# Performance work log

Hardware: AMD Instinct MI355X
Metric: run time of the kernel (lower is better)

The kernel has to match this reference:

```python
import jax, jax.numpy as jnp
import numpy as np

T = 1.0  # temperature

def _free_energy(v, W, b, c):
    # v: [B, V]; W: [V, H]; b: [V]; c: [H]
    vW = v @ W                                  # [B, H]
    W_colsum = W.sum(axis=0)                    # [H]
    negF_normal = (v * b).sum(-1) - jax.nn.softplus(vW + c).sum(-1)
    negF_flip = ((1.0 - v) * b).sum(-1) - jax.nn.softplus(W_colsum - vW + c).sum(-1)
    negF = jnp.stack([negF_normal, negF_flip], axis=-1)  # [B, 2]
    return -T * jax.nn.logsumexp(negF / T, axis=-1)      # [B]

def _gibbs_chain(v0, W, b, c, key, k):
    B = v0.shape[0]
    key, k0 = jax.random.split(key)
    u0 = jax.random.bernoulli(k0, 0.5, (B, 1)).astype(v0.dtype)
    b_sum = b.sum()

    def step(carry, _):
        v, u, key = carry
        key, k1, k2, k3 = jax.random.split(key, 4)
        v_branch = u * v + (1.0 - u) * (1.0 - v)
        h = jax.random.bernoulli(k1, jax.nn.sigmoid(v_branch @ W + c)).astype(v.dtype)  # [B,H]
        a = h @ W.T                                                                     # [B,V]
        vb = (v * b).sum(-1)
        va = (v * a).sum(-1)
        dE = -b_sum - a.sum(-1) + 2.0 * vb + 2.0 * va
        u_new = jax.random.bernoulli(k2, jax.nn.sigmoid(dE)).astype(v.dtype)[:, None]
        v_new = jax.random.bernoulli(k3, jax.nn.sigmoid(a + b)).astype(v.dtype)
        v = u_new * v_new + (1.0 - u_new) * (1.0 - v_new)
        return (v, u_new, key), None

    (v_model, _, _), _ = jax.lax.scan(step, (v0, u0, key), None, length=k)
    return v_model

def setup_inputs() -> dict:
    key = jax.random.key(0)
    kv, kw = jax.random.split(key)
    B, V, H = 8192, 1024, 1024
    v_data = jnp.round(jax.random.uniform(kv, (B, V), dtype=jnp.float32))  # binary 0/1
    W = 0.01 * jax.random.normal(kw, (V, H), dtype=jnp.float32)
    b = jnp.zeros((V,), dtype=jnp.float32)
    c = jnp.zeros((H,), dtype=jnp.float32)
    return {"v_data": v_data, "W": W, "b": b, "c": c, "seed": 0}

def reference(v_data, W, b, c, seed):
    K = 10  # Gibbs steps
    key = jax.random.key(seed)
    v_model = _gibbs_chain(v_data, W, b, c, key, K)
    v_model = jax.lax.stop_gradient(v_model)  # .detach() in torch
    loss = _free_energy(v_data, W, b, c).mean() - _free_energy(v_model, W, b, c).mean()
    return loss
```

## Files before the change

### kernel.cpp

```cpp
#include <hip/hip_runtime.h>
#include <hip/hip_bf16.h>
#include <stdint.h>
#include <math.h>


static constexpr int Bn = 8192;
static constexpr int Vn = 1024;
static constexpr int Hn = 1024;
static constexpr int KSTEPS = 10;

typedef _Float16 f16;
typedef f16   f16x4 __attribute__((ext_vector_type(4)));
typedef f16   f16x8 __attribute__((ext_vector_type(8)));
typedef float f32x4 __attribute__((ext_vector_type(4)));

#define GLOBAL_LOAD_LDS16(g, l)                                              \
  __builtin_amdgcn_global_load_lds(                                          \
      (const __attribute__((address_space(1))) uint32_t*)(g),                \
      (__attribute__((address_space(3))) uint32_t*)(l), 16, 0, 0)

__device__ __forceinline__ uint32_t rotl32(uint32_t x, int d) {
  return (x << d) | (x >> (32 - d));
}

__device__ __forceinline__ void tf2x32(uint32_t k0, uint32_t k1,
                                       uint32_t x0, uint32_t x1,
                                       uint32_t& o0, uint32_t& o1) {
  uint32_t k2 = k0 ^ k1 ^ 0x1BD11BDAu;
#define TFR(r) { x0 += x1; x1 = rotl32(x1, (r)); x1 ^= x0; }
  x0 += k0; x1 += k1;
  TFR(13) TFR(15) TFR(26) TFR(6)
  x0 += k1; x1 += k2 + 1u;
  TFR(17) TFR(29) TFR(16) TFR(24)
  x0 += k2; x1 += k0 + 2u;
  TFR(13) TFR(15) TFR(26) TFR(6)
  x0 += k0; x1 += k1 + 3u;
  TFR(17) TFR(29) TFR(16) TFR(24)
  x0 += k1; x1 += k2 + 4u;
  TFR(13) TFR(15) TFR(26) TFR(6)
  x0 += k2; x1 += k0 + 5u;
#undef TFR
  o0 = x0; o1 = x1;
}

__device__ __forceinline__ float rng_u01(uint2 key, uint32_t idx) {
  uint32_t o0, o1;
  tf2x32(key.x, key.y, 0u, idx, o0, o1);
  uint32_t bits = o0 ^ o1;
  return __uint_as_float((bits >> 9) | 0x3F800000u) - 1.0f;
}

__device__ __forceinline__ float bern_fast(float z, float r01) {
  float e = __expf(-z);
  return (__builtin_fmaf(r01, e, r01) < 1.0f) ? 1.f : 0.f;
}
__device__ __forceinline__ float softplus_fast(float x) {
  return fmaxf(x, 0.f) + __logf(1.f + __expf(-fabsf(x)));
}

__global__ void prep_keys(const int* __restrict__ seedp, uint2* __restrict__ keys) {
  if (threadIdx.x != 0 || blockIdx.x != 0) return;
  uint32_t seed = (uint32_t)(*seedp);
  uint2 key = make_uint2(0u, seed);
  uint2 nk, kk;
  tf2x32(key.x, key.y, 0u, 0u, nk.x, nk.y);
  tf2x32(key.x, key.y, 0u, 1u, kk.x, kk.y);
  keys[0] = kk;
  key = nk;
  for (int s = 0; s < KSTEPS; ++s) {
    uint2 t0, t1, t2, t3;
    tf2x32(key.x, key.y, 0u, 0u, t0.x, t0.y);
    tf2x32(key.x, key.y, 0u, 1u, t1.x, t1.y);
    tf2x32(key.x, key.y, 0u, 2u, t2.x, t2.y);
    tf2x32(key.x, key.y, 0u, 3u, t3.x, t3.y);
    key = t0;
    keys[1 + 3*s] = t1;
    keys[2 + 3*s] = t2;
    keys[3 + 3*s] = t3;
  }
}

__global__ __launch_bounds__(256) void colsum_part(
    const float* __restrict__ W, float* __restrict__ part) {
  const int bx = blockIdx.x, t = threadIdx.x;
  float s0 = 0.f, s1 = 0.f, s2 = 0.f, s3 = 0.f;
#pragma unroll
  for (int r = 0; r < 16; ++r) {
    const float* row = W + (size_t)(bx * 16 + r) * Hn;
    s0 += row[t]; s1 += row[t + 256]; s2 += row[t + 512]; s3 += row[t + 768];
  }
  float* p = part + (size_t)bx * Hn;
  p[t] = s0; p[t + 256] = s1; p[t + 512] = s2; p[t + 768] = s3;
}

__global__ __launch_bounds__(256) void colsum_red(
    const float* __restrict__ part, float* __restrict__ cs) {
  const int col = blockIdx.x * 256 + threadIdx.x;
  float s = 0.f;
#pragma unroll
  for (int k = 0; k < 64; ++k) s += part[(size_t)k * Hn + col];
  cs[col] = s;
}

__global__ void bsum_k(const float* __restrict__ bvec, float* __restrict__ bs) {
  __shared__ float sb[4];
  float s = 0.f;
  for (int i = threadIdx.x; i < Vn; i += 256) s += bvec[i];
  for (int off = 32; off > 0; off >>= 1) s += __shfl_down(s, off, 64);
  int wv = threadIdx.x >> 6, ln = threadIdx.x & 63;
  if (ln == 0) sb[wv] = s;
  __syncthreads();
  if (threadIdx.x == 0) bs[0] = sb[0] + sb[1] + sb[2] + sb[3];
}

__global__ __launch_bounds__(256) void cast_W(
    const float* __restrict__ W, f16* __restrict__ Wf, f16* __restrict__ WTf) {
  __shared__ f16 tile[64][65];
  const int j0 = blockIdx.x * 64, i0 = blockIdx.y * 64;
  const int tx = threadIdx.x & 63, tg = threadIdx.x >> 6;
#pragma unroll 4
  for (int rr = 0; rr < 16; ++rr) {
    const int row = tg * 16 + rr;
    float w = W[(size_t)(i0 + row) * Hn + j0 + tx];
    f16 hw = (f16)w;
    Wf[(size_t)(i0 + row) * Hn + j0 + tx] = hw;
    tile[row][tx] = hw;
  }
  __syncthreads();
#pragma unroll 4
  for (int rr = 0; rr < 16; ++rr) {
    const int row = tg * 16 + rr;
    WTf[(size_t)(j0 + row) * Vn + i0 + tx] = tile[tx][row];
  }
}

__global__ void u0_init(const uint2* __restrict__ keys, float* __restrict__ u) {
  int b = blockIdx.x * 256 + threadIdx.x;
  float r01 = rng_u01(keys[0], (uint32_t)b);
  u[b] = (r01 < 0.5f) ? 1.f : 0.f;
}

__global__ __launch_bounds__(256) void cast_vx(
    const float* __restrict__ vd, const float* __restrict__ u,
    f16* __restrict__ x) {
  const int idx = blockIdx.x * 256 + threadIdx.x;
  const int row = idx >> 8;
  const float uo = u[row];
  const float4 d = ((const float4*)vd)[idx];
  f16x4 o;
  if (uo > 0.5f) { o[0]=(f16)d.x; o[1]=(f16)d.y; o[2]=(f16)d.z; o[3]=(f16)d.w; }
  else { o[0]=(f16)(1.f-d.x); o[1]=(f16)(1.f-d.y); o[2]=(f16)(1.f-d.z); o[3]=(f16)(1.f-d.w); }
  *(f16x4*)(x + (size_t)idx * 4) = o;
}

template <int EPI>
__global__ __launch_bounds__(256, 8) void gemm_s(
    const f16* __restrict__ A, const f16* __restrict__ Bm,
    f16* __restrict__ outA, f16* __restrict__ outH,
    const f16* __restrict__ xold, f16* __restrict__ xnew,
    const float* __restrict__ bvec, const float* __restrict__ cvec,
    float* __restrict__ pA, float* __restrict__ pXA, float* __restrict__ pXB,
    const uint2* __restrict__ keys, int keyIdx)
{
  constexpr int N = 1024, K = 1024, BK = 64;
  __shared__ alignas(16) f16 As[64 * BK];
  __shared__ alignas(16) f16 Bs[64 * BK];

  const int t = threadIdx.x, wave = t >> 6, lane = t & 63;
  const int l15 = lane & 15, quad = lane >> 4;
  const int m0 = blockIdx.x * 64, n0 = blockIdx.y * 64;
  const int wm = (wave >> 1) * 32, wn = (wave & 1) * 32;

  const int rbase = lane >> 3;
  const int gch   = (lane & 7) ^ rbase;
  const f16* gA = A  + (size_t)(m0 + wave * 16 + rbase) * K + gch * 8;
  const f16* gB = Bm + (size_t)(n0 + wave * 16 + rbase) * K + gch * 8;
  f16* lA = As + wave * 16 * BK;
  f16* lB = Bs + wave * 16 * BK;

  const int swz = l15 & 7;
  const int oA  = (wm + l15) * BK;
  const int oB  = (wn + l15) * BK;

  f32x4 acc[2][2] = {};

  for (int k0 = 0; k0 < K; k0 += BK) {
    GLOBAL_LOAD_LDS16(gA + k0,         lA);
    GLOBAL_LOAD_LDS16(gA + k0 + 8 * K, lA + 8 * BK);
    GLOBAL_LOAD_LDS16(gB + k0,         lB);
    GLOBAL_LOAD_LDS16(gB + k0 + 8 * K, lB + 8 * BK);
    __syncthreads();

#pragma unroll
    for (int kc = 0; kc < 2; ++kc) {
      const int fc = ((kc * 4 + quad) ^ swz) * 8;
      f16x8 af[2], bf[2];
#pragma unroll
      for (int i = 0; i < 2; ++i) {
        af[i] = *(const f16x8*)(&As[oA + i * 16 * BK + fc]);
        bf[i] = *(const f16x8*)(&Bs[oB + i * 16 * BK + fc]);
      }
#pragma unroll
      for (int mt = 0; mt < 2; ++mt)
#pragma unroll
        for (int nt = 0; nt < 2; ++nt)
          acc[mt][nt] = __builtin_amdgcn_mfma_f32_16x16x32_f16(af[mt], bf[nt], acc[mt][nt], 0, 0, 0);
    }
    __syncthreads();
  }

  if constexpr (EPI == 0 || EPI == 1 || EPI == 2) {
    const uint2 key = (EPI != 0) ? keys[keyIdx] : make_uint2(0u, 0u);
#pragma unroll
    for (int mt = 0; mt < 2; ++mt)
#pragma unroll
      for (int r = 0; r < 4; ++r) {
        const int gm = m0 + wm + mt * 16 + quad * 4 + r;
#pragma unroll
        for (int nt = 0; nt < 2; ++nt) {
          const int gn = n0 + wn + nt * 16 + l15;
          const float val = acc[mt][nt][r];
          if constexpr (EPI == 0 || EPI == 2)
            outA[(size_t)gm * N + gn] = (f16)val;
          if constexpr (EPI == 1 || EPI == 2) {
            float z   = val + cvec[gn];
            float r01 = rng_u01(key, (uint32_t)(gm * N + gn));
            outH[(size_t)gm * N + gn] = (f16)bern_fast(z, r01);
          }
        }
      }
  } else {
    const uint2 key = keys[keyIdx];
    float bb[2];
#pragma unroll
    for (int nt = 0; nt < 2; ++nt) bb[nt] = bvec[n0 + wn + nt * 16 + l15];
#pragma unroll
    for (int mt = 0; mt < 2; ++mt)
#pragma unroll
      for (int r = 0; r < 4; ++r) {
        const int gm = m0 + wm + mt * 16 + quad * 4 + r;
        float pa = 0.f, pxa = 0.f, pxb = 0.f;
#pragma unroll
        for (int nt = 0; nt < 2; ++nt) {
          const int gn = n0 + wn + nt * 16 + l15;
          const float aval = acc[mt][nt][r];
          const float xo   = (float)xold[(size_t)gm * N + gn];
          pa  += aval;
          pxa += xo * aval;
          pxb += xo * bb[nt];
          float r01 = rng_u01(key, (uint32_t)(gm * N + gn));
          xnew[(size_t)gm * N + gn] = (f16)bern_fast(aval + bb[nt], r01);
        }
#pragma unroll
        for (int m = 1; m < 16; m <<= 1) {
          pa  += __shfl_xor(pa,  m, 64);
          pxa += __shfl_xor(pxa, m, 64);
          pxb += __shfl_xor(pxb, m, 64);
        }
        if (l15 == 0) {
          const int slot = blockIdx.y * 2 + (wave & 1);
          pA [(size_t)gm * 32 + slot] = pa;
          pXA[(size_t)gm * 32 + slot] = pxa;
          pXB[(size_t)gm * 32 + slot] = pxb;
        }
      }
  }
}

__global__ __launch_bounds__(256) void u_chain(
    const float* __restrict__ pA, const float* __restrict__ pXA,
    const float* __restrict__ pXB, const float* __restrict__ bsum,
    const uint2* __restrict__ keys, float* __restrict__ u)
{
  const int t = threadIdx.x, wave = t >> 6, lane = t & 63;
  const int r2 = lane >> 5, slot = lane & 31;
  const int row = blockIdx.x * 8 + wave * 2 + r2;
  const float bs = bsum[0];
  float uo = u[row];
  for (int s = 0; s < KSTEPS; ++s) {
    const size_t o = (size_t)s * 32 * Bn + (size_t)row * 32 + slot;
    float sa  = pA [o];
    float sxa = pXA[o];
    float sxb = pXB[o];
#pragma unroll
    for (int m = 1; m < 32; m <<= 1) {
      sa  += __shfl_xor(sa,  m, 64);
      sxa += __shfl_xor(sxa, m, 64);
      sxb += __shfl_xor(sxb, m, 64);
    }
    const float va = (uo > 0.5f) ? sxa : sa - sxa;
    const float vb = (uo > 0.5f) ? sxb : bs - sxb;
    const float dE = -bs - sa + 2.f * vb + 2.f * va;
    uo = bern_fast(dE, rng_u01(keys[2 + 3 * s], (uint32_t)row));
  }
  if (slot == 0) u[row] = uo;
}

__global__ __launch_bounds__(256) void fe_rows(
    const f16* __restrict__ araw, const f16* __restrict__ x,
    const float* __restrict__ u,
    const float* __restrict__ bvec, const float* __restrict__ cvec,
    const float* __restrict__ colsum, const float* __restrict__ bsum,
    float* __restrict__ Fout)
{
  __shared__ float s1[4], s2[4], s3[4];
  const int row = blockIdx.x;
  const int t = threadIdx.x;
  const float uo = u[row];
  const f16x4  a4 = *(const f16x4*)(araw + (size_t)row * Hn + t * 4);
  const float4 c4 = ((const float4*)cvec)[t];
  const float4 w4 = ((const float4*)colsum)[t];
  const float4 b4 = ((const float4*)bvec)[t];
  const f16x4  x4 = *(const f16x4*)(x + (size_t)row * Vn + t * 4);

  float aa[4] = { (float)a4[0], (float)a4[1], (float)a4[2], (float)a4[3] };
  float cc[4] = { c4.x, c4.y, c4.z, c4.w };
  float ww[4] = { w4.x, w4.y, w4.z, w4.w };
  float bb[4] = { b4.x, b4.y, b4.z, b4.w };
  float S1 = 0.f, S2 = 0.f, xb = 0.f;
#pragma unroll
  for (int j = 0; j < 4; ++j) {
    float m = (uo > 0.5f) ? aa[j] : ww[j] - aa[j];
    S1 += softplus_fast(m + cc[j]);
    S2 += softplus_fast(ww[j] - m + cc[j]);
    xb += (float)x4[j] * bb[j];
  }
#pragma unroll
  for (int off = 32; off > 0; off >>= 1) {
    S1 += __shfl_down(S1, off, 64);
    S2 += __shfl_down(S2, off, 64);
    xb += __shfl_down(xb, off, 64);
  }
  const int wv = t >> 6, ln = t & 63;
  if (ln == 0) { s1[wv] = S1; s2[wv] = S2; s3[wv] = xb; }
  __syncthreads();
  if (t == 0) {
    S1 = s1[0] + s1[1] + s1[2] + s1[3];
    S2 = s2[0] + s2[1] + s2[2] + s2[3];
    xb = s3[0] + s3[1] + s3[2] + s3[3];
    float vb = (uo > 0.5f) ? xb : bsum[0] - xb;
    float negn = vb - S1;
    float negf = (bsum[0] - vb) - S2;
    float mx = fmaxf(negn, negf);
    Fout[row] = -(mx + logf(expf(negn - mx) + expf(negf - mx)));
  }
}

__global__ __launch_bounds__(256) void finalize_k(
    const float* __restrict__ Fd, const float* __restrict__ Fm, float* __restrict__ out)
{
  __shared__ double sb[8];
  double sd = 0.0, sm = 0.0;
  for (int i = threadIdx.x; i < Bn; i += 256) { sd += (double)Fd[i]; sm += (double)Fm[i]; }
  for (int off = 32; off > 0; off >>= 1) { sd += __shfl_down(sd, off, 64); sm += __shfl_down(sm, off, 64); }
  const int wv = threadIdx.x >> 6, ln = threadIdx.x & 63;
  if (ln == 0) { sb[wv] = sd; sb[4 + wv] = sm; }
  __syncthreads();
  if (threadIdx.x == 0) {
    sd = sb[0] + sb[1] + sb[2] + sb[3];
    sm = sb[4] + sb[5] + sb[6] + sb[7];
    out[0] = (float)((sd - sm) / (double)Bn);
  }
}

extern "C" void kernel_launch(void* const* d_in, const int* in_sizes, int n_in,
                              void* d_out, int out_size, void* d_ws, size_t ws_size,
                              hipStream_t stream) {
  const float* v_data = (const float*)d_in[0];
  const float* W      = (const float*)d_in[1];
  const float* bvec   = (const float*)d_in[2];
  const float* cvec   = (const float*)d_in[3];
  const int*   seedp  = (const int*)d_in[4];
  float* out = (float*)d_out;

  char* ws = (char*)d_ws;
  size_t off = 0;
  auto alloc = [&](size_t bytes) -> void* {
    void* p = ws + off;
    off += (bytes + 255) & ~(size_t)255;
    return p;
  };
  f16*   xb0  = (f16*)alloc((size_t)Bn * Vn * 2);
  f16*   xb1  = (f16*)alloc((size_t)Bn * Vn * 2);
  f16*   h    = (f16*)alloc((size_t)Bn * Hn * 2);
  f16*   araw = (f16*)alloc((size_t)Bn * Hn * 2);
  f16*   Wf   = (f16*)alloc((size_t)Vn * Hn * 2);
  f16*   WTf  = (f16*)alloc((size_t)Vn * Hn * 2);
  float* cpart  = (float*)alloc(64 * Hn * 4);
  float* colsum = (float*)alloc(Hn * 4);
  float* bsum   = (float*)alloc(256);
  uint2* keys   = (uint2*)alloc(64 * sizeof(uint2));
  float* u      = (float*)alloc(Bn * 4);
  float* pA     = (float*)alloc((size_t)KSTEPS * 32 * Bn * 4);
  float* pXA    = (float*)alloc((size_t)KSTEPS * 32 * Bn * 4);
  float* pXB    = (float*)alloc((size_t)KSTEPS * 32 * Bn * 4);
  float* Fd     = (float*)alloc(Bn * 4);
  float* Fm     = (float*)alloc(Bn * 4);
  (void)ws_size; (void)in_sizes; (void)n_in; (void)out_size;

  prep_keys<<<1, 64, 0, stream>>>(seedp, keys);
  colsum_part<<<64, 256, 0, stream>>>(W, cpart);
  colsum_red<<<4, 256, 0, stream>>>(cpart, colsum);
  bsum_k<<<1, 256, 0, stream>>>(bvec, bsum);
  cast_W<<<dim3(Hn / 64, Vn / 64), 256, 0, stream>>>(W, Wf, WTf);
  u0_init<<<Bn / 256, 256, 0, stream>>>(keys, u);
  cast_vx<<<(Bn * Vn / 4) / 256, 256, 0, stream>>>(v_data, u, xb0);

  dim3 gg(Bn / 64, Hn / 64);
  f16* xs[2] = { xb0, xb1 };

  gemm_s<2><<<gg, 256, 0, stream>>>(xb0, WTf, araw, h, nullptr, nullptr,
                                    nullptr, cvec, nullptr, nullptr, nullptr, keys, 1);
  fe_rows<<<Bn, 256, 0, stream>>>(araw, xb0, u, bvec, cvec, colsum, bsum, Fd);

  for (int s = 0; s < KSTEPS; ++s) {
    if (s > 0) {
      gemm_s<1><<<gg, 256, 0, stream>>>(xs[s & 1], WTf, nullptr, h, nullptr,
                                        nullptr, nullptr, cvec, nullptr, nullptr,
                                        nullptr, keys, 1 + 3 * s);
    }
    const size_t so = (size_t)s * 32 * Bn;
    gemm_s<3><<<gg, 256, 0, stream>>>(h, Wf, nullptr, nullptr, xs[s & 1],
                                      xs[(s + 1) & 1], bvec, nullptr,
                                      pA + so, pXA + so, pXB + so, keys, 3 + 3 * s);
  }

  gemm_s<0><<<gg, 256, 0, stream>>>(xs[KSTEPS & 1], WTf, araw, nullptr, nullptr,
                                    nullptr, nullptr, nullptr, nullptr, nullptr,
                                    nullptr, keys, 0);
  u_chain<<<Bn / 8, 256, 0, stream>>>(pA, pXA, pXB, bsum, keys, u);
  fe_rows<<<Bn, 256, 0, stream>>>(araw, xs[KSTEPS & 1], u, bvec, cvec, colsum, bsum, Fm);

  finalize_k<<<1, 256, 0, stream>>>(Fd, Fm, out);
}
```

Measured before the change: 947.2 us.

## Fuse free-energy softplus sums and u-chain partials into GEMM epilogues

The free-energy softplus reductions move into the epilogues of the first and final v@W GEMMs, which removes the raw activation buffer write and the separate fe_rows passes. The u-chain partial sums are reformulated as h·colsum and h·(vW), computed in the h-sampling epilogue, so the W^T GEMM epilogue no longer reads the old x. The x·b partials are computed where x is produced, including in the cast kernel. This removes several full B×H fp16 reads and writes, at the cost of heavier epilogues with more transcendentals and extra partial-sum buffers.

Result: no change. 941.0 us (-0.7%).

```diff
diff --git a/kernel.cpp b/kernel.cpp
--- a/kernel.cpp
+++ b/kernel.cpp
@@ -134,32 +134,39 @@
   }
 }
 
-__global__ void u0_init(const uint2* __restrict__ keys, float* __restrict__ u) {
+__global__ void u0_init(const uint2* __restrict__ keys, float* __restrict__ u0) {
   int b = blockIdx.x * 256 + threadIdx.x;
   float r01 = rng_u01(keys[0], (uint32_t)b);
-  u[b] = (r01 < 0.5f) ? 1.f : 0.f;
+  u0[b] = (r01 < 0.5f) ? 1.f : 0.f;
 }
 
 __global__ __launch_bounds__(256) void cast_vx(
-    const float* __restrict__ vd, const float* __restrict__ u,
-    f16* __restrict__ x) {
-  const int idx = blockIdx.x * 256 + threadIdx.x;
-  const int row = idx >> 8;
-  const float uo = u[row];
-  const float4 d = ((const float4*)vd)[idx];
-  f16x4 o;
-  if (uo > 0.5f) { o[0]=(f16)d.x; o[1]=(f16)d.y; o[2]=(f16)d.z; o[3]=(f16)d.w; }
-  else { o[0]=(f16)(1.f-d.x); o[1]=(f16)(1.f-d.y); o[2]=(f16)(1.f-d.z); o[3]=(f16)(1.f-d.w); }
-  *(f16x4*)(x + (size_t)idx * 4) = o;
+    const float* __restrict__ vd, const float* __restrict__ u0,
+    const float* __restrict__ bvec, f16* __restrict__ x,
+    float* __restrict__ pXB0) {
+  const int row = blockIdx.x;
+  const int t = threadIdx.x;
+  const float uo = u0[row];
+  const float4 d  = ((const float4*)(vd + (size_t)row * Vn))[t];
+  const float4 bv = ((const float4*)bvec)[t];
+  float xv[4] = { d.x, d.y, d.z, d.w };
+  if (uo <= 0.5f) { xv[0]=1.f-xv[0]; xv[1]=1.f-xv[1]; xv[2]=1.f-xv[2]; xv[3]=1.f-xv[3]; }
+  f16x4 o = { (f16)xv[0], (f16)xv[1], (f16)xv[2], (f16)xv[3] };
+  *(f16x4*)(x + (size_t)row * Vn + t * 4) = o;
+  float xb = xv[0]*bv.x + xv[1]*bv.y + xv[2]*bv.z + xv[3]*bv.w;
+#pragma unroll
+  for (int m = 1; m < 8; m <<= 1) xb += __shfl_xor(xb, m, 64);
+  if ((t & 7) == 0) pXB0[(size_t)row * 32 + (t >> 3)] = xb;
 }
 
 template <int EPI>
 __global__ __launch_bounds__(256, 8) void gemm_s(
     const f16* __restrict__ A, const f16* __restrict__ Bm,
-    f16* __restrict__ outA, f16* __restrict__ outH,
-    const f16* __restrict__ xold, f16* __restrict__ xnew,
+    f16* __restrict__ outH, f16* __restrict__ xnew,
     const float* __restrict__ bvec, const float* __restrict__ cvec,
-    float* __restrict__ pA, float* __restrict__ pXA, float* __restrict__ pXB,
+    const float* __restrict__ colsum,
+    float* __restrict__ pA, float* __restrict__ pXA, float* __restrict__ pXBn,
+    float* __restrict__ pSA, float* __restrict__ pSB,
     const uint2* __restrict__ keys, int keyIdx)
 {
   constexpr int N = 1024, K = 1024, BK = 64;
@@ -209,27 +216,56 @@
     __syncthreads();
   }
 
-  if constexpr (EPI == 0 || EPI == 1 || EPI == 2) {
-    const uint2 key = (EPI != 0) ? keys[keyIdx] : make_uint2(0u, 0u);
+  const int slot = blockIdx.y * 2 + (wave & 1);
+
+  if constexpr (EPI == 1 || EPI == 2) {
+    const uint2 key = keys[keyIdx];
+    float csv[2], cvv[2];
+#pragma unroll
+    for (int nt = 0; nt < 2; ++nt) {
+      const int gn = n0 + wn + nt * 16 + l15;
+      csv[nt] = colsum[gn];
+      cvv[nt] = cvec[gn];
+    }
 #pragma unroll
     for (int mt = 0; mt < 2; ++mt)
 #pragma unroll
       for (int r = 0; r < 4; ++r) {
         const int gm = m0 + wm + mt * 16 + quad * 4 + r;
+        float pa = 0.f, pxa = 0.f, sa = 0.f, sb = 0.f;
 #pragma unroll
         for (int nt = 0; nt < 2; ++nt) {
           const int gn = n0 + wn + nt * 16 + l15;
           const float val = acc[mt][nt][r];
-          if constexpr (EPI == 0 || EPI == 2)
-            outA[(size_t)gm * N + gn] = (f16)val;
-          if constexpr (EPI == 1 || EPI == 2) {
-            float z   = val + cvec[gn];
-            float r01 = rng_u01(key, (uint32_t)(gm * N + gn));
-            outH[(size_t)gm * N + gn] = (f16)bern_fast(z, r01);
+          float r01 = rng_u01(key, (uint32_t)(gm * N + gn));
+          float hq  = bern_fast(val + cvv[nt], r01);
+          outH[(size_t)gm * N + gn] = (f16)hq;
+          pa  += hq * csv[nt];
+          pxa += hq * val;
+          if constexpr (EPI == 2) {
+            sa += softplus_fast(val + cvv[nt]);
+            sb += softplus_fast(csv[nt] - val + cvv[nt]);
           }
         }
+#pragma unroll
+        for (int m = 1; m < 16; m <<= 1) {
+          pa  += __shfl_xor(pa,  m, 64);
+          pxa += __shfl_xor(pxa, m, 64);
+          if constexpr (EPI == 2) {
+            sa += __shfl_xor(sa, m, 64);
+            sb += __shfl_xor(sb, m, 64);
+          }
+        }
+        if (l15 == 0) {
+          pA [(size_t)gm * 32 + slot] = pa;
+          pXA[(size_t)gm * 32 + slot] = pxa;
+          if constexpr (EPI == 2) {
+            pSA[(size_t)gm * 32 + slot] = sa;
+            pSB[(size_t)gm * 32 + slot] = sb;
+          }
+        }
       }
-  } else {
+  } else if constexpr (EPI == 3) {
     const uint2 key = keys[keyIdx];
     float bb[2];
 #pragma unroll
@@ -239,29 +275,48 @@
 #pragma unroll
       for (int r = 0; r < 4; ++r) {
         const int gm = m0 + wm + mt * 16 + quad * 4 + r;
-        float pa = 0.f, pxa = 0.f, pxb = 0.f;
+        float pxb = 0.f;
 #pragma unroll
         for (int nt = 0; nt < 2; ++nt) {
           const int gn = n0 + wn + nt * 16 + l15;
           const float aval = acc[mt][nt][r];
-          const float xo   = (float)xold[(size_t)gm * N + gn];
-          pa  += aval;
-          pxa += xo * aval;
-          pxb += xo * bb[nt];
           float r01 = rng_u01(key, (uint32_t)(gm * N + gn));
-          xnew[(size_t)gm * N + gn] = (f16)bern_fast(aval + bb[nt], r01);
+          float xq  = bern_fast(aval + bb[nt], r01);
+          xnew[(size_t)gm * N + gn] = (f16)xq;
+          pxb += xq * bb[nt];
+        }
+#pragma unroll
+        for (int m = 1; m < 16; m <<= 1) pxb += __shfl_xor(pxb, m, 64);
+        if (l15 == 0) pXBn[(size_t)gm * 32 + slot] = pxb;
+      }
+  } else {
+    float csv[2], cvv[2];
+#pragma unroll
+    for (int nt = 0; nt < 2; ++nt) {
+      const int gn = n0 + wn + nt * 16 + l15;
+      csv[nt] = colsum[gn];
+      cvv[nt] = cvec[gn];
+    }
+#pragma unroll
+    for (int mt = 0; mt < 2; ++mt)
+#pragma unroll
+      for (int r = 0; r < 4; ++r) {
+        const int gm = m0 + wm + mt * 16 + quad * 4 + r;
+        float sa = 0.f, sb = 0.f;
+#pragma unroll
+        for (int nt = 0; nt < 2; ++nt) {
+          const float val = acc[mt][nt][r];
+          sa += softplus_fast(val + cvv[nt]);
+          sb += softplus_fast(csv[nt] - val + cvv[nt]);
         }
 #pragma unroll
         for (int m = 1; m < 16; m <<= 1) {
-          pa  += __shfl_xor(pa,  m, 64);
-          pxa += __shfl_xor(pxa, m, 64);
-          pxb += __shfl_xor(pxb, m, 64);
+          sa += __shfl_xor(sa, m, 64);
+          sb += __shfl_xor(sb, m, 64);
         }
         if (l15 == 0) {
-          const int slot = blockIdx.y * 2 + (wave & 1);
-          pA [(size_t)gm * 32 + slot] = pa;
-          pXA[(size_t)gm * 32 + slot] = pxa;
-          pXB[(size_t)gm * 32 + slot] = pxb;
+          pSA[(size_t)gm * 32 + slot] = sa;
+          pSB[(size_t)gm * 32 + slot] = sb;
         }
       }
   }
@@ -270,13 +325,14 @@
 __global__ __launch_bounds__(256) void u_chain(
     const float* __restrict__ pA, const float* __restrict__ pXA,
     const float* __restrict__ pXB, const float* __restrict__ bsum,
-    const uint2* __restrict__ keys, float* __restrict__ u)
+    const uint2* __restrict__ keys, const float* __restrict__ u0,
+    float* __restrict__ uF)
 {
   const int t = threadIdx.x, wave = t >> 6, lane = t & 63;
   const int r2 = lane >> 5, slot = lane & 31;
   const int row = blockIdx.x * 8 + wave * 2 + r2;
   const float bs = bsum[0];
-  float uo = u[row];
+  float uo = u0[row];
   for (int s = 0; s < KSTEPS; ++s) {
     const size_t o = (size_t)s * 32 * Bn + (size_t)row * 32 + slot;
     float sa  = pA [o];
@@ -293,56 +349,45 @@
     const float dE = -bs - sa + 2.f * vb + 2.f * va;
     uo = bern_fast(dE, rng_u01(keys[2 + 3 * s], (uint32_t)row));
   }
-  if (slot == 0) u[row] = uo;
-}
-
-__global__ __launch_bounds__(256) void fe_rows(
-    const f16* __restrict__ araw, const f16* __restrict__ x,
-    const float* __restrict__ u,
-    const float* __restrict__ bvec, const float* __restrict__ cvec,
-    const float* __restrict__ colsum, const float* __restrict__ bsum,
-    float* __restrict__ Fout)
+  if (slot == 0) uF[row] = uo;
+}
+
+__device__ __forceinline__ float fe_eval(float SA, float SB, float xb,
+                                         float uo, float bs) {
+  float S1 = (uo > 0.5f) ? SA : SB;
+  float S2 = (uo > 0.5f) ? SB : SA;
+  float vb = (uo > 0.5f) ? xb : bs - xb;
+  float negn = vb - S1;
+  float negf = (bs - vb) - S2;
+  float mx = fmaxf(negn, negf);
+  return -(mx + logf(expf(negn - mx) + expf(negf - mx)));
+}
+
+__global__ __launch_bounds__(256) void fe_finish(
+    const float* __restrict__ SA0, const float* __restrict__ SB0,
+    const float* __restrict__ xb0,
+    const float* __restrict__ SAF, const float* __restrict__ SBF,
+    const float* __restrict__ xbF,
+    const float* __restrict__ u0, const float* __restrict__ uF,
+    const float* __restrict__ bsum,
+    float* __restrict__ Fd, float* __restrict__ Fm)
 {
-  __shared__ float s1[4], s2[4], s3[4];
-  const int row = blockIdx.x;
-  const int t = threadIdx.x;
-  const float uo = u[row];
-  const f16x4  a4 = *(const f16x4*)(araw + (size_t)row * Hn + t * 4);
-  const float4 c4 = ((const float4*)cvec)[t];
-  const float4 w4 = ((const float4*)colsum)[t];
-  const float4 b4 = ((const float4*)bvec)[t];
-  const f16x4  x4 = *(const f16x4*)(x + (size_t)row * Vn + t * 4);
-
-  float aa[4] = { (float)a4[0], (float)a4[1], (float)a4[2], (float)a4[3] };
-  float cc[4] = { c4.x, c4.y, c4.z, c4.w };
-  float ww[4] = { w4.x, w4.y, w4.z, w4.w };
-  float bb[4] = { b4.x, b4.y, b4.z, b4.w };
-  float S1 = 0.f, S2 = 0.f, xb = 0.f;
-#pragma unroll
-  for (int j = 0; j < 4; ++j) {
-    float m = (uo > 0.5f) ? aa[j] : ww[j] - aa[j];
-    S1 += softplus_fast(m + cc[j]);
-    S2 += softplus_fast(ww[j] - m + cc[j]);
-    xb += (float)x4[j] * bb[j];
-  }
-#pragma unroll
-  for (int off = 32; off > 0; off >>= 1) {
-    S1 += __shfl_down(S1, off, 64);
-    S2 += __shfl_down(S2, off, 64);
-    xb += __shfl_down(xb, off, 64);
-  }
-  const int wv = t >> 6, ln = t & 63;
-  if (ln == 0) { s1[wv] = S1; s2[wv] = S2; s3[wv] = xb; }
-  __syncthreads();
-  if (t == 0) {
-    S1 = s1[0] + s1[1] + s1[2] + s1[3];
-    S2 = s2[0] + s2[1] + s2[2] + s2[3];
-    xb = s3[0] + s3[1] + s3[2] + s3[3];
-    float vb = (uo > 0.5f) ? xb : bsum[0] - xb;
-    float negn = vb - S1;
-    float negf = (bsum[0] - vb) - S2;
-    float mx = fmaxf(negn, negf);
-    Fout[row] = -(mx + logf(expf(negn - mx) + expf(negf - mx)));
+  const int t = threadIdx.x, wave = t >> 6, lane = t & 63;
+  const int r2 = lane >> 5, slot = lane & 31;
+  const int row = blockIdx.x * 8 + wave * 2 + r2;
+  const size_t o = (size_t)row * 32 + slot;
+  const float bs = bsum[0];
+  float a0 = SA0[o], b0 = SB0[o], x0 = xb0[o];
+  float aF = SAF[o], bF = SBF[o], xF = xbF[o];
+#pragma unroll
+  for (int m = 1; m < 32; m <<= 1) {
+    a0 += __shfl_xor(a0, m, 64);  b0 += __shfl_xor(b0, m, 64);
+    x0 += __shfl_xor(x0, m, 64);  aF += __shfl_xor(aF, m, 64);
+    bF += __shfl_xor(bF, m, 64);  xF += __shfl_xor(xF, m, 64);
+  }
+  if (slot == 0) {
+    Fd[row] = fe_eval(a0, b0, x0, u0[row], bs);
+    Fm[row] = fe_eval(aF, bF, xF, uF[row], bs);
   }
 }
 
@@ -383,17 +428,21 @@
   f16*   xb0  = (f16*)alloc((size_t)Bn * Vn * 2);
   f16*   xb1  = (f16*)alloc((size_t)Bn * Vn * 2);
   f16*   h    = (f16*)alloc((size_t)Bn * Hn * 2);
-  f16*   araw = (f16*)alloc((size_t)Bn * Hn * 2);
   f16*   Wf   = (f16*)alloc((size_t)Vn * Hn * 2);
   f16*   WTf  = (f16*)alloc((size_t)Vn * Hn * 2);
   float* cpart  = (float*)alloc(64 * Hn * 4);
   float* colsum = (float*)alloc(Hn * 4);
   float* bsum   = (float*)alloc(256);
   uint2* keys   = (uint2*)alloc(64 * sizeof(uint2));
-  float* u      = (float*)alloc(Bn * 4);
+  float* u0     = (float*)alloc(Bn * 4);
+  float* uF     = (float*)alloc(Bn * 4);
   float* pA     = (float*)alloc((size_t)KSTEPS * 32 * Bn * 4);
   float* pXA    = (float*)alloc((size_t)KSTEPS * 32 * Bn * 4);
-  float* pXB    = (float*)alloc((size_t)KSTEPS * 32 * Bn * 4);
+  float* pXB    = (float*)alloc((size_t)(KSTEPS + 1) * 32 * Bn * 4);
+  float* SA0    = (float*)alloc((size_t)32 * Bn * 4);
+  float* SB0    = (float*)alloc((size_t)32 * Bn * 4);
+  float* SAF    = (float*)alloc((size_t)32 * Bn * 4);
+  float* SBF    = (float*)alloc((size_t)32 * Bn * 4);
   float* Fd     = (float*)alloc(Bn * 4);
   float* Fm     = (float*)alloc(Bn * 4);
   (void)ws_size; (void)in_sizes; (void)n_in; (void)out_size;
@@ -403,33 +452,37 @@
   colsum_red<<<4, 256, 0, stream>>>(cpart, colsum);
   bsum_k<<<1, 256, 0, stream>>>(bvec, bsum);
   cast_W<<<dim3(Hn / 64, Vn / 64), 256, 0, stream>>>(W, Wf, WTf);
-  u0_init<<<Bn / 256, 256, 0, stream>>>(keys, u);
-  cast_vx<<<(Bn * Vn / 4) / 256, 256, 0, stream>>>(v_data, u, xb0);
+  u0_init<<<Bn / 256, 256, 0, stream>>>(keys, u0);
+  cast_vx<<<Bn, 256, 0, stream>>>(v_data, u0, bvec, xb0, pXB);
 
   dim3 gg(Bn / 64, Hn / 64);
   f16* xs[2] = { xb0, xb1 };
-
-  gemm_s<2><<<gg, 256, 0, stream>>>(xb0, WTf, araw, h, nullptr, nullptr,
-                                    nullptr, cvec, nullptr, nullptr, nullptr, keys, 1);
-  fe_rows<<<Bn, 256, 0, stream>>>(araw, xb0, u, bvec, cvec, colsum, bsum, Fd);
+  const size_t SL = (size_t)32 * Bn;
 
   for (int s = 0; s < KSTEPS; ++s) {
-    if (s > 0) {
-      gemm_s<1><<<gg, 256, 0, stream>>>(xs[s & 1], WTf, nullptr, h, nullptr,
-                                        nullptr, nullptr, cvec, nullptr, nullptr,
-                                        nullptr, keys, 1 + 3 * s);
+    if (s == 0) {
+      gemm_s<2><<<gg, 256, 0, stream>>>(xs[0], WTf, h, nullptr, nullptr, cvec,
+                                        colsum, pA, pXA, nullptr, SA0, SB0,
+                                        keys, 1);
+    } else {
+      gemm_s<1><<<gg, 256, 0, stream>>>(xs[s & 1], WTf, h, nullptr, nullptr, cvec,
+                                        colsum, pA + (size_t)s * SL,
+                                        pXA + (size_t)s * SL, nullptr,
+                                        nullptr, nullptr, keys, 1 + 3 * s);
     }
-    const size_t so = (size_t)s * 32 * Bn;
-    gemm_s<3><<<gg, 256, 0, stream>>>(h, Wf, nullptr, nullptr, xs[s & 1],
-                                      xs[(s + 1) & 1], bvec, nullptr,
-                                      pA + so, pXA + so, pXB + so, keys, 3 + 3 * s);
-  }
-
-  gemm_s<0><<<gg, 256, 0, stream>>>(xs[KSTEPS & 1], WTf, araw, nullptr, nullptr,
-                                    nullptr, nullptr, nullptr, nullptr, nullptr,
-                                    nullptr, keys, 0);
-  u_chain<<<Bn / 8, 256, 0, stream>>>(pA, pXA, pXB, bsum, keys, u);
-  fe_rows<<<Bn, 256, 0, stream>>>(araw, xs[KSTEPS & 1], u, bvec, cvec, colsum, bsum, Fm);
-
+    gemm_s<3><<<gg, 256, 0, stream>>>(h, Wf, nullptr, xs[(s + 1) & 1], bvec,
+                                      nullptr, nullptr, nullptr, nullptr,
+                                      pXB + (size_t)(s + 1) * SL,
+                                      nullptr, nullptr, keys, 3 + 3 * s);
+  }
+
+  gemm_s<4><<<gg, 256, 0, stream>>>(xs[KSTEPS & 1], WTf, nullptr, nullptr,
+                                    nullptr, cvec, colsum, nullptr, nullptr,
+                                    nullptr, SAF, SBF, keys, 0);
+
+  u_chain<<<Bn / 8, 256, 0, stream>>>(pA, pXA, pXB, bsum, keys, u0, uF);
+  fe_finish<<<Bn / 8, 256, 0, stream>>>(SA0, SB0, pXB,
+                                        SAF, SBF, pXB + (size_t)KSTEPS * SL,
+                                        u0, uF, bsum, Fd, Fm);
   finalize_k<<<1, 256, 0, stream>>>(Fd, Fm, out);
 }
```
